# Performance work log

Measured on AMD Instinct MI355X. Metric: run time of the kernel, lower is better.

## Reference

```python
import jax, jax.numpy as jnp
import numpy as np

TOP_K = 2


def setup_inputs() -> dict:
    key = jax.random.key(0)
    k1, k2, k3, k4, k5 = jax.random.split(key, 5)
    B, S, H, F, E = 2, 2048, 1024, 4096, 8
    scale = 0.02
    return {
        "hidden_states": jax.random.normal(k1, (B, S, H), dtype=jnp.float32),
        "w_gate": jax.random.normal(k2, (H, E), dtype=jnp.float32) * scale,
        "w_gate_proj": jax.random.normal(k3, (E, H, F), dtype=jnp.float32) * scale,
        "w_up_proj": jax.random.normal(k4, (E, H, F), dtype=jnp.float32) * scale,
        "w_down_proj": jax.random.normal(k5, (E, F, H), dtype=jnp.float32) * scale,
    }


def reference(hidden_states, w_gate, w_gate_proj, w_up_proj, w_down_proj):
    B, S, H = hidden_states.shape
    E = w_gate_proj.shape[0]
    x = hidden_states.reshape(-1, H)  # [T, H]

    # Router: softmax in float32, then top-k (NOT renormalized, matching source).
    router_logits = x @ w_gate  # [T, E]
    routing_probs = jax.nn.softmax(router_logits.astype(jnp.float32), axis=-1)
    routing_weights, selected_experts = jax.lax.top_k(routing_probs, TOP_K)  # [T, k]
    routing_weights = routing_weights.astype(x.dtype)

    out = jnp.zeros_like(x)
    # Small fixed loop over experts; per-token weight is zero for unrouted
    # tokens, so the masked dense computation is mathematically identical to
    # the gather/index_add dispatch in the source.
    for e in range(E):
        w_e = jnp.sum(routing_weights * (selected_experts == e), axis=-1)  # [T]
        h = jax.nn.silu(x @ w_gate_proj[e]) * (x @ w_up_proj[e])  # [T, F]
        out = out + (h @ w_down_proj[e]) * w_e[:, None]
    return out.reshape(B, S, H)
```

## Files before the change

### kernel.cpp

```cpp
#include <hip/hip_runtime.h>
#include <hip/hip_bf16.h>

#define T_TOK 4096
#define HDIM  1024
#define FDIM  4096
#define NEXP  8
#define CAP   4096
#define NTMAX 64
#define OBR   8192

typedef __attribute__((ext_vector_type(8))) short short8;
typedef __attribute__((ext_vector_type(4))) float floatx4;
typedef __attribute__((ext_vector_type(4))) float float4v;
typedef __attribute__((ext_vector_type(4))) unsigned short ushort4v;

__device__ __forceinline__ unsigned short f2bf(float f) {
    union { float f; unsigned int u; } v; v.f = f;
    unsigned int u = v.u;
    u += 0x7fffu + ((u >> 16) & 1u);
    return (unsigned short)(u >> 16);
}

__device__ __forceinline__ void gl2lds16(const void* g, void* l) {
    __builtin_amdgcn_global_load_lds(
        (const __attribute__((address_space(1))) unsigned int*)g,
        (__attribute__((address_space(3))) unsigned int*)l,
        16, 0, 0);
}

__global__ void k_transpose_cast(const float* __restrict__ src, unsigned short* __restrict__ dst,
                                 int R, int C) {
    __shared__ float tile[64][65];
    size_t base = (size_t)blockIdx.z * (size_t)R * (size_t)C;
    int c0 = blockIdx.x * 64, r0 = blockIdx.y * 64;
    int lx = threadIdx.x & 15, ly = threadIdx.x >> 4;
#pragma unroll
    for (int i = 0; i < 4; ++i) {
        int rr = i * 16 + ly;
        float4v v = *(const float4v*)(src + base + (size_t)(r0 + rr) * C + c0 + lx * 4);
        tile[rr][lx * 4 + 0] = v[0]; tile[rr][lx * 4 + 1] = v[1];
        tile[rr][lx * 4 + 2] = v[2]; tile[rr][lx * 4 + 3] = v[3];
    }
    __syncthreads();
#pragma unroll
    for (int i = 0; i < 4; ++i) {
        int cc = i * 16 + ly;
        ushort4v o = { f2bf(tile[lx * 4 + 0][cc]), f2bf(tile[lx * 4 + 1][cc]),
                       f2bf(tile[lx * 4 + 2][cc]), f2bf(tile[lx * 4 + 3][cc]) };
        *(ushort4v*)(dst + base + (size_t)(c0 + cc) * R + r0 + lx * 4) = o;
    }
}

__global__ void k_transpose_cast2(const float* __restrict__ s0, const float* __restrict__ s1,
                                  unsigned short* __restrict__ d0, unsigned short* __restrict__ d1) {
    const int R = HDIM, C = FDIM;
    __shared__ float tile[64][65];
    int m = blockIdx.z >> 3, zz = blockIdx.z & 7;
    const float* src = (m ? s1 : s0);
    unsigned short* dst = (m ? d1 : d0);
    size_t base = (size_t)zz * (size_t)R * (size_t)C;
    int c0 = blockIdx.x * 64, r0 = blockIdx.y * 64;
    int lx = threadIdx.x & 15, ly = threadIdx.x >> 4;
#pragma unroll
    for (int i = 0; i < 4; ++i) {
        int rr = i * 16 + ly;
        float4v v = *(const float4v*)(src + base + (size_t)(r0 + rr) * C + c0 + lx * 4);
        tile[rr][lx * 4 + 0] = v[0]; tile[rr][lx * 4 + 1] = v[1];
        tile[rr][lx * 4 + 2] = v[2]; tile[rr][lx * 4 + 3] = v[3];
    }
    __syncthreads();
#pragma unroll
    for (int i = 0; i < 4; ++i) {
        int cc = i * 16 + ly;
        ushort4v o = { f2bf(tile[lx * 4 + 0][cc]), f2bf(tile[lx * 4 + 1][cc]),
                       f2bf(tile[lx * 4 + 2][cc]), f2bf(tile[lx * 4 + 3][cc]) };
        *(ushort4v*)(dst + base + (size_t)(c0 + cc) * R + r0 + lx * 4) = o;
    }
}

__global__ void k_router(const float* __restrict__ x, const float* __restrict__ wgate,
                         unsigned short* __restrict__ xb,
                         int* __restrict__ counts, int* __restrict__ ltok,
                         float* __restrict__ lwt, int* __restrict__ tslot) {
    int lane = threadIdx.x & 63;
    int tok = blockIdx.x * 4 + (threadIdx.x >> 6);
    const float* xr = x + (size_t)tok * HDIM;
    unsigned short* xbr = xb + (size_t)tok * HDIM;
    float acc[NEXP];
#pragma unroll
    for (int e = 0; e < NEXP; ++e) acc[e] = 0.f;
    for (int it = 0; it < HDIM / 256; ++it) {
        int h0 = it * 256 + lane * 4;
        float4v xv = *(const float4v*)(xr + h0);
        ushort4v xo = { f2bf(xv[0]), f2bf(xv[1]), f2bf(xv[2]), f2bf(xv[3]) };
        *(ushort4v*)(xbr + h0) = xo;
#pragma unroll
        for (int j = 0; j < 4; ++j) {
            float4v w0 = *(const float4v*)(wgate + (size_t)(h0 + j) * NEXP);
            float4v w1 = *(const float4v*)(wgate + (size_t)(h0 + j) * NEXP + 4);
            float xs = xv[j];
            acc[0] += xs * w0[0]; acc[1] += xs * w0[1];
            acc[2] += xs * w0[2]; acc[3] += xs * w0[3];
            acc[4] += xs * w1[0]; acc[5] += xs * w1[1];
            acc[6] += xs * w1[2]; acc[7] += xs * w1[3];
        }
    }
#pragma unroll
    for (int off = 32; off >= 1; off >>= 1)
#pragma unroll
        for (int e = 0; e < NEXP; ++e)
            acc[e] += __shfl_xor(acc[e], off, 64);
    if (lane == 0) {
        float m = acc[0];
#pragma unroll
        for (int e = 1; e < NEXP; ++e) m = fmaxf(m, acc[e]);
        float p[NEXP], s = 0.f;
#pragma unroll
        for (int e = 0; e < NEXP; ++e) { p[e] = __expf(acc[e] - m); s += p[e]; }
        float inv = 1.f / s;
#pragma unroll
        for (int e = 0; e < NEXP; ++e) p[e] *= inv;
        int e0 = 0; float b0 = p[0];
#pragma unroll
        for (int e = 1; e < NEXP; ++e) if (p[e] > b0) { b0 = p[e]; e0 = e; }
        int e1 = -1; float b1 = -1.f;
#pragma unroll
        for (int e = 0; e < NEXP; ++e) if (e != e0 && p[e] > b1) { b1 = p[e]; e1 = e; }
        int p0 = atomicAdd(&counts[e0], 1);
        ltok[e0 * CAP + p0] = tok; lwt[e0 * CAP + p0] = b0;
        int p1 = atomicAdd(&counts[e1], 1);
        ltok[e1 * CAP + p1] = tok; lwt[e1 * CAP + p1] = b1;
        tslot[tok * 2]     = (e0 << 16) | p0;
        tslot[tok * 2 + 1] = (e1 << 16) | p1;
    }
}

__global__ void k_prefix(const int* __restrict__ counts, int* __restrict__ offs,
                         int* __restrict__ wl, int* __restrict__ nwl) {
    if (threadIdx.x == 0) {
        int s = 0;
#pragma unroll
        for (int e = 0; e < NEXP; ++e) { offs[e] = s; s += counts[e]; }
        int n = 0;
        for (int e = 0; e < NEXP; ++e)
            for (int r = 0; r * 256 < counts[e] && n < NTMAX; ++r)
                wl[n++] = (e << 8) | r;
        nwl[0] = n;
    }
}

__global__ __launch_bounds__(512, 4)
void k_gemm1(const unsigned short* __restrict__ xb,
             const unsigned short* __restrict__ wgt,
             const unsigned short* __restrict__ wut,
             const int* __restrict__ counts, const int* __restrict__ offs,
             const int* __restrict__ ltok,
             const int* __restrict__ wl, const int* __restrict__ nwl,
             unsigned short* __restrict__ hbuf)
{
    const int bid = blockIdx.x;
    const int ftile = bid & 63;
    const int by = bid >> 6;
    if (by >= nwl[0]) return;
    const int w = wl[by];
    const int e = w >> 8, rowtile = w & 255;
    const int M = counts[e];

    __shared__ __align__(16) unsigned short lA[2][256 * 32];
    __shared__ __align__(16) unsigned short lBg[2][64 * 32];
    __shared__ __align__(16) unsigned short lBu[2][64 * 32];
    __shared__ int stok[256];

    const int t = threadIdx.x;
    const int wv = t >> 6, lane = t & 63;

    if (t < 256) {
        int i = rowtile * 256 + t;
        stok[t] = (i < M) ? ltok[e * CAP + i] : ltok[e * CAP];
    }
    __syncthreads();

    const int srow = wv * 16 + (lane >> 2);
    const int k4 = lane & 3;
    const int swA = (k4 ^ ((srow >> 1) & 3)) * 8;
    const unsigned short* pA0 = xb + (size_t)stok[srow] * HDIM + swA;
    const unsigned short* pA1 = xb + (size_t)stok[128 + srow] * HDIM + swA;
    const int brow = (wv & 3) * 16 + (lane >> 2);
    const int swB = (k4 ^ ((brow >> 1) & 3)) * 8;
    const unsigned short* wsrc = (wv < 4) ? wgt : wut;
    const unsigned short* pB = wsrc + ((size_t)e * FDIM + ftile * 64 + brow) * HDIM + swB;

    const int wm = wv >> 1, wn = wv & 1;
    const int fr = lane & 15, kg = lane >> 4;
    const int cswz = (kg ^ ((fr >> 1) & 3)) * 8;

    floatx4 accg[4][2], accu[4][2];
#pragma unroll
    for (int mi = 0; mi < 4; ++mi)
#pragma unroll
        for (int ni = 0; ni < 2; ++ni) {
            floatx4 z = {0.f, 0.f, 0.f, 0.f};
            accg[mi][ni] = z; accu[mi][ni] = z;
        }

    auto stage = [&](int b) {
        gl2lds16(pA0, &lA[b][wv * 512]);        pA0 += 32;
        gl2lds16(pA1, &lA[b][4096 + wv * 512]); pA1 += 32;
        gl2lds16(pB, (wv < 4) ? &lBg[b][(wv & 3) * 512]
                              : &lBu[b][(wv & 3) * 512]);
        pB += 32;
    };
    auto compute = [&](int b) {
        short8 a[4], g[2], u[2];
#pragma unroll
        for (int mi = 0; mi < 4; ++mi)
            a[mi] = *(const short8*)&lA[b][(wm * 64 + mi * 16 + fr) * 32 + cswz];
#pragma unroll
        for (int ni = 0; ni < 2; ++ni) {
            g[ni] = *(const short8*)&lBg[b][(wn * 32 + ni * 16 + fr) * 32 + cswz];
            u[ni] = *(const short8*)&lBu[b][(wn * 32 + ni * 16 + fr) * 32 + cswz];
        }
#pragma unroll
        for (int mi = 0; mi < 4; ++mi)
#pragma unroll
            for (int ni = 0; ni < 2; ++ni) {
                accg[mi][ni] = __builtin_amdgcn_mfma_f32_16x16x32_bf16(a[mi], g[ni], accg[mi][ni], 0, 0, 0);
                accu[mi][ni] = __builtin_amdgcn_mfma_f32_16x16x32_bf16(a[mi], u[ni], accu[mi][ni], 0, 0, 0);
            }
    };

    stage(0);
    __syncthreads();
#pragma unroll 1
    for (int it = 0; it < 16; ++it) {
        stage(1);
        compute(0);
        __syncthreads();
        if (it < 15) stage(0);
        compute(1);
        __syncthreads();
    }

    const int hrow0 = offs[e] + rowtile * 256;
#pragma unroll
    for (int mi = 0; mi < 4; ++mi)
#pragma unroll
        for (int ni = 0; ni < 2; ++ni) {
            int c = ftile * 64 + wn * 32 + ni * 16 + fr;
#pragma unroll
            for (int r = 0; r < 4; ++r) {
                int rr = wm * 64 + mi * 16 + kg * 4 + r;
                if (rowtile * 256 + rr < M) {
                    float g = accg[mi][ni][r];
                    float val = (g / (1.f + __expf(-g))) * accu[mi][ni][r];
                    hbuf[(size_t)(hrow0 + rr) * FDIM + c] = f2bf(val);
                }
            }
        }
}

__global__ __launch_bounds__(512, 4)
void k_gemm2(const unsigned short* __restrict__ hbuf,
             const unsigned short* __restrict__ wdt,
             const int* __restrict__ counts, const int* __restrict__ offs,
             const float* __restrict__ lwt,
             const int* __restrict__ wl, const int* __restrict__ nwl,
             float* __restrict__ obuf)
{
    const int bid = blockIdx.x;
    const int htile = bid & 7;
    const int kq = (bid >> 3) & 3;
    const int by = bid >> 5;
    if (by >= nwl[0]) return;
    const int w = wl[by];
    const int e = w >> 8, rowtile = w & 255;
    const int M = counts[e];

    __shared__ __align__(16) unsigned short lA[2][256 * 32];
    __shared__ __align__(16) unsigned short lB[2][128 * 32];
    __shared__ float swt[256];

    const int t = threadIdx.x;
    const int wv = t >> 6, lane = t & 63;

    if (t < 256) {
        int i = rowtile * 256 + t;
        swt[t] = (i < M) ? lwt[e * CAP + i] : 0.f;
    }

    const int row0 = offs[e] + rowtile * 256;
    const int srow = wv * 16 + (lane >> 2);
    const int k4 = lane & 3;
    const int sw = (k4 ^ ((srow >> 1) & 3)) * 8;
    const int kofs = kq * (FDIM / 4);
    const int ra0 = min(row0 + srow, OBR - 1);
    const int ra1 = min(row0 + 128 + srow, OBR - 1);
    const unsigned short* pA0 = hbuf + (size_t)ra0 * FDIM + kofs + sw;
    const unsigned short* pA1 = hbuf + (size_t)ra1 * FDIM + kofs + sw;
    const unsigned short* pB = wdt + ((size_t)e * HDIM + htile * 128 + srow) * FDIM + kofs + sw;

    const int wm = wv >> 1, wn = wv & 1;
    const int fr = lane & 15, kg = lane >> 4;
    const int cswz = (kg ^ ((fr >> 1) & 3)) * 8;

    floatx4 acc[4][4];
#pragma unroll
    for (int mi = 0; mi < 4; ++mi)
#pragma unroll
        for (int ni = 0; ni < 4; ++ni) {
            floatx4 z = {0.f, 0.f, 0.f, 0.f};
            acc[mi][ni] = z;
        }

    auto stage = [&](int b) {
        gl2lds16(pA0, &lA[b][wv * 512]);        pA0 += 32;
        gl2lds16(pA1, &lA[b][4096 + wv * 512]); pA1 += 32;
        gl2lds16(pB,  &lB[b][wv * 512]);        pB += 32;
    };
    auto compute = [&](int b) {
        short8 a[4], bb[4];
#pragma unroll
        for (int mi = 0; mi < 4; ++mi)
            a[mi] = *(const short8*)&lA[b][(wm * 64 + mi * 16 + fr) * 32 + cswz];
#pragma unroll
        for (int ni = 0; ni < 4; ++ni)
            bb[ni] = *(const short8*)&lB[b][(wn * 64 + ni * 16 + fr) * 32 + cswz];
#pragma unroll
        for (int mi = 0; mi < 4; ++mi)
#pragma unroll
            for (int ni = 0; ni < 4; ++ni)
                acc[mi][ni] = __builtin_amdgcn_mfma_f32_16x16x32_bf16(a[mi], bb[ni], acc[mi][ni], 0, 0, 0);
    };

    stage(0);
    __syncthreads();
#pragma unroll 1
    for (int it = 0; it < 16; ++it) {
        stage(1);
        compute(0);
        __syncthreads();
        if (it < 15) stage(0);
        compute(1);
        __syncthreads();
    }

    float* ob = obuf + (size_t)kq * OBR * HDIM;
#pragma unroll
    for (int mi = 0; mi < 4; ++mi)
#pragma unroll
        for (int ni = 0; ni < 4; ++ni) {
            int c = htile * 128 + wn * 64 + ni * 16 + fr;
#pragma unroll
            for (int r = 0; r < 4; ++r) {
                int rr = wm * 64 + mi * 16 + kg * 4 + r;
                if (rowtile * 256 + rr < M)
                    ob[(size_t)(row0 + rr) * HDIM + c] = acc[mi][ni][r] * swt[rr];
            }
        }
}

__global__ void k_combine(const float* __restrict__ obuf, const int* __restrict__ tslot,
                          const int* __restrict__ offs, float* __restrict__ out) {
    int gid = blockIdx.x * 256 + threadIdx.x;
    int tok = gid >> 8;
    int c = (gid & 255) * 4;
    int s0 = tslot[tok * 2], s1 = tslot[tok * 2 + 1];
    size_t r0 = (size_t)(offs[s0 >> 16] + (s0 & 0xFFFF));
    size_t r1 = (size_t)(offs[s1 >> 16] + (s1 & 0xFFFF));
    float4v s = {0.f, 0.f, 0.f, 0.f};
#pragma unroll
    for (int q = 0; q < 4; ++q) {
        s += *(const float4v*)(obuf + ((size_t)q * OBR + r0) * HDIM + c);
        s += *(const float4v*)(obuf + ((size_t)q * OBR + r1) * HDIM + c);
    }
    *(float4v*)(out + (size_t)tok * HDIM + c) = s;
}

extern "C" void kernel_launch(void* const* d_in, const int* in_sizes, int n_in,
                              void* d_out, int out_size, void* d_ws, size_t ws_size,
                              hipStream_t stream) {
    const float* x     = (const float*)d_in[0];
    const float* wgate = (const float*)d_in[1];
    const float* wg    = (const float*)d_in[2];
    const float* wu    = (const float*)d_in[3];
    const float* wd    = (const float*)d_in[4];
    float* out = (float*)d_out;

    char* ws = (char*)d_ws;
    size_t off = 0;
    unsigned short* xb  = (unsigned short*)(ws + off); off += (size_t)T_TOK * HDIM * 2;
    unsigned short* wgt = (unsigned short*)(ws + off); off += (size_t)NEXP * FDIM * HDIM * 2;
    unsigned short* wut = (unsigned short*)(ws + off); off += (size_t)NEXP * FDIM * HDIM * 2;
    unsigned short* wdt = (unsigned short*)(ws + off); off += (size_t)NEXP * HDIM * FDIM * 2;
    unsigned short* hbuf= (unsigned short*)(ws + off); off += (size_t)OBR * FDIM * 2;
    int*   ltok   = (int*)(ws + off);   off += (size_t)NEXP * CAP * 4;
    float* lwt    = (float*)(ws + off); off += (size_t)NEXP * CAP * 4;
    int*   tslot  = (int*)(ws + off);   off += (size_t)T_TOK * 2 * 4;
    int*   counts = (int*)(ws + off);   off += 256;
    int*   offs   = (int*)(ws + off);   off += 256;
    int*   wl     = (int*)(ws + off);   off += NTMAX * 4;
    int*   nwl    = (int*)(ws + off);   off += 256;
    float* obuf = (float*)wgt;

    hipMemsetAsync(counts, 0, 32, stream);

    k_router<<<T_TOK / 4, 256, 0, stream>>>(x, wgate, xb, counts, ltok, lwt, tslot);
    k_transpose_cast2<<<dim3(FDIM / 64, HDIM / 64, 16), 256, 0, stream>>>(wg, wu, wgt, wut);
    k_transpose_cast<<<dim3(HDIM / 64, FDIM / 64, NEXP), 256, 0, stream>>>(wd, wdt, FDIM, HDIM);
    k_prefix<<<1, 64, 0, stream>>>(counts, offs, wl, nwl);
    k_gemm1<<<64 * 40, 512, 0, stream>>>(xb, wgt, wut, counts, offs, ltok, wl, nwl, hbuf);
    k_gemm2<<<32 * 40, 512, 0, stream>>>(hbuf, wdt, counts, offs, lwt, wl, nwl, obuf);
    k_combine<<<T_TOK * HDIM / 1024, 256, 0, stream>>>(obuf, tslot, offs, out);
}
```

Baseline: 827.6 us.

## Fuse fp32 weight cast and transpose into GEMM B-tile staging

```diff
diff --git a/kernel.cpp b/kernel.cpp
--- a/kernel.cpp
+++ b/kernel.cpp
@@ -12,6 +12,7 @@
 typedef __attribute__((ext_vector_type(8))) short short8;
 typedef __attribute__((ext_vector_type(4))) float floatx4;
 typedef __attribute__((ext_vector_type(4))) float float4v;
+typedef __attribute__((ext_vector_type(2))) float float2v;
 typedef __attribute__((ext_vector_type(4))) unsigned short ushort4v;
 
 __device__ __forceinline__ unsigned short f2bf(float f) {
@@ -26,56 +27,6 @@
         (const __attribute__((address_space(1))) unsigned int*)g,
         (__attribute__((address_space(3))) unsigned int*)l,
         16, 0, 0);
-}
-
-__global__ void k_transpose_cast(const float* __restrict__ src, unsigned short* __restrict__ dst,
-                                 int R, int C) {
-    __shared__ float tile[64][65];
-    size_t base = (size_t)blockIdx.z * (size_t)R * (size_t)C;
-    int c0 = blockIdx.x * 64, r0 = blockIdx.y * 64;
-    int lx = threadIdx.x & 15, ly = threadIdx.x >> 4;
-#pragma unroll
-    for (int i = 0; i < 4; ++i) {
-        int rr = i * 16 + ly;
-        float4v v = *(const float4v*)(src + base + (size_t)(r0 + rr) * C + c0 + lx * 4);
-        tile[rr][lx * 4 + 0] = v[0]; tile[rr][lx * 4 + 1] = v[1];
-        tile[rr][lx * 4 + 2] = v[2]; tile[rr][lx * 4 + 3] = v[3];
-    }
-    __syncthreads();
-#pragma unroll
-    for (int i = 0; i < 4; ++i) {
-        int cc = i * 16 + ly;
-        ushort4v o = { f2bf(tile[lx * 4 + 0][cc]), f2bf(tile[lx * 4 + 1][cc]),
-                       f2bf(tile[lx * 4 + 2][cc]), f2bf(tile[lx * 4 + 3][cc]) };
-        *(ushort4v*)(dst + base + (size_t)(c0 + cc) * R + r0 + lx * 4) = o;
-    }
-}
-
-__global__ void k_transpose_cast2(const float* __restrict__ s0, const float* __restrict__ s1,
-                                  unsigned short* __restrict__ d0, unsigned short* __restrict__ d1) {
-    const int R = HDIM, C = FDIM;
-    __shared__ float tile[64][65];
-    int m = blockIdx.z >> 3, zz = blockIdx.z & 7;
-    const float* src = (m ? s1 : s0);
-    unsigned short* dst = (m ? d1 : d0);
-    size_t base = (size_t)zz * (size_t)R * (size_t)C;
-    int c0 = blockIdx.x * 64, r0 = blockIdx.y * 64;
-    int lx = threadIdx.x & 15, ly = threadIdx.x >> 4;
-#pragma unroll
-    for (int i = 0; i < 4; ++i) {
-        int rr = i * 16 + ly;
-        float4v v = *(const float4v*)(src + base + (size_t)(r0 + rr) * C + c0 + lx * 4);
-        tile[rr][lx * 4 + 0] = v[0]; tile[rr][lx * 4 + 1] = v[1];
-        tile[rr][lx * 4 + 2] = v[2]; tile[rr][lx * 4 + 3] = v[3];
-    }
-    __syncthreads();
-#pragma unroll
-    for (int i = 0; i < 4; ++i) {
-        int cc = i * 16 + ly;
-        ushort4v o = { f2bf(tile[lx * 4 + 0][cc]), f2bf(tile[lx * 4 + 1][cc]),
-                       f2bf(tile[lx * 4 + 2][cc]), f2bf(tile[lx * 4 + 3][cc]) };
-        *(ushort4v*)(dst + base + (size_t)(c0 + cc) * R + r0 + lx * 4) = o;
-    }
 }
 
 __global__ void k_router(const float* __restrict__ x, const float* __restrict__ wgate,
@@ -151,8 +102,8 @@
 
 __global__ __launch_bounds__(512, 4)
 void k_gemm1(const unsigned short* __restrict__ xb,
-             const unsigned short* __restrict__ wgt,
-             const unsigned short* __restrict__ wut,
+             const float* __restrict__ wg,
+             const float* __restrict__ wu,
              const int* __restrict__ counts, const int* __restrict__ offs,
              const int* __restrict__ ltok,
              const int* __restrict__ wl, const int* __restrict__ nwl,
@@ -185,10 +136,13 @@
     const int swA = (k4 ^ ((srow >> 1) & 3)) * 8;
     const unsigned short* pA0 = xb + (size_t)stok[srow] * HDIM + swA;
     const unsigned short* pA1 = xb + (size_t)stok[128 + srow] * HDIM + swA;
-    const int brow = (wv & 3) * 16 + (lane >> 2);
-    const int swB = (k4 ^ ((brow >> 1) & 3)) * 8;
-    const unsigned short* wsrc = (wv < 4) ? wgt : wut;
-    const unsigned short* pB = wsrc + ((size_t)e * FDIM + ftile * 64 + brow) * HDIM + swB;
+
+    const int tt = t & 255;
+    const int bn0 = 2 * (tt & 31);
+    const int bk0 = 4 * (tt >> 5);
+    const float* wsrc = (wv < 4) ? wg : wu;
+    const float* pB = wsrc + (size_t)e * HDIM * FDIM + (size_t)bk0 * FDIM + ftile * 64 + bn0;
+    const int wo0 = bn0 * 32 + (((bk0 >> 3) ^ ((bn0 >> 1) & 3)) << 3) + (bk0 & 7);
 
     const int wm = wv >> 1, wn = wv & 1;
     const int fr = lane & 15, kg = lane >> 4;
@@ -203,12 +157,24 @@
             accg[mi][ni] = z; accu[mi][ni] = z;
         }
 
-    auto stage = [&](int b) {
+    float2v q0, q1, q2, q3;
+    auto ldB = [&]() {
+        q0 = *(const float2v*)(pB);
+        q1 = *(const float2v*)(pB + FDIM);
+        q2 = *(const float2v*)(pB + 2 * FDIM);
+        q3 = *(const float2v*)(pB + 3 * FDIM);
+        pB += 32 * FDIM;
+    };
+    auto writeB = [&](int b) {
+        unsigned short* base = ((wv < 4) ? &lBg[b][0] : &lBu[b][0]) + wo0;
+        ushort4v lo = { f2bf(q0[0]), f2bf(q1[0]), f2bf(q2[0]), f2bf(q3[0]) };
+        ushort4v hi = { f2bf(q0[1]), f2bf(q1[1]), f2bf(q2[1]), f2bf(q3[1]) };
+        *(ushort4v*)(base) = lo;
+        *(ushort4v*)(base + 32) = hi;
+    };
+    auto stageA = [&](int b) {
         gl2lds16(pA0, &lA[b][wv * 512]);        pA0 += 32;
         gl2lds16(pA1, &lA[b][4096 + wv * 512]); pA1 += 32;
-        gl2lds16(pB, (wv < 4) ? &lBg[b][(wv & 3) * 512]
-                              : &lBu[b][(wv & 3) * 512]);
-        pB += 32;
     };
     auto compute = [&](int b) {
         short8 a[4], g[2], u[2];
@@ -229,15 +195,17 @@
             }
     };
 
-    stage(0);
+    ldB();
+    stageA(0);
+    writeB(0);
     __syncthreads();
+
 #pragma unroll 1
-    for (int it = 0; it < 16; ++it) {
-        stage(1);
-        compute(0);
-        __syncthreads();
-        if (it < 15) stage(0);
-        compute(1);
+    for (int it = 0; it < 32; ++it) {
+        const int b = it & 1;
+        if (it < 31) { ldB(); stageA(b ^ 1); }
+        compute(b);
+        if (it < 31) writeB(b ^ 1);
         __syncthreads();
     }
 
@@ -261,7 +229,7 @@
 
 __global__ __launch_bounds__(512, 4)
 void k_gemm2(const unsigned short* __restrict__ hbuf,
-             const unsigned short* __restrict__ wdt,
+             const float* __restrict__ wd,
              const int* __restrict__ counts, const int* __restrict__ offs,
              const float* __restrict__ lwt,
              const int* __restrict__ wl, const int* __restrict__ nwl,
@@ -289,15 +257,20 @@
     }
 
     const int row0 = offs[e] + rowtile * 256;
+
     const int srow = wv * 16 + (lane >> 2);
     const int k4 = lane & 3;
-    const int sw = (k4 ^ ((srow >> 1) & 3)) * 8;
+    const int swA = (k4 ^ ((srow >> 1) & 3)) * 8;
     const int kofs = kq * (FDIM / 4);
     const int ra0 = min(row0 + srow, OBR - 1);
     const int ra1 = min(row0 + 128 + srow, OBR - 1);
-    const unsigned short* pA0 = hbuf + (size_t)ra0 * FDIM + kofs + sw;
-    const unsigned short* pA1 = hbuf + (size_t)ra1 * FDIM + kofs + sw;
-    const unsigned short* pB = wdt + ((size_t)e * HDIM + htile * 128 + srow) * FDIM + kofs + sw;
+    const unsigned short* pA0 = hbuf + (size_t)ra0 * FDIM + kofs + swA;
+    const unsigned short* pA1 = hbuf + (size_t)ra1 * FDIM + kofs + swA;
+
+    const int bn0 = 2 * (t & 63);
+    const int bk0 = 4 * wv;
+    const float* pB = wd + (size_t)e * FDIM * HDIM + (size_t)(kofs + bk0) * HDIM + htile * 128 + bn0;
+    const int wo0 = bn0 * 32 + (((bk0 >> 3) ^ ((bn0 >> 1) & 3)) << 3) + (bk0 & 7);
 
     const int wm = wv >> 1, wn = wv & 1;
     const int fr = lane & 15, kg = lane >> 4;
@@ -312,10 +285,24 @@
             acc[mi][ni] = z;
         }
 
-    auto stage = [&](int b) {
+    float2v q0, q1, q2, q3;
+    auto ldB = [&]() {
+        q0 = *(const float2v*)(pB);
+        q1 = *(const float2v*)(pB + HDIM);
+        q2 = *(const float2v*)(pB + 2 * HDIM);
+        q3 = *(const float2v*)(pB + 3 * HDIM);
+        pB += 32 * HDIM;
+    };
+    auto writeB = [&](int b) {
+        unsigned short* base = &lB[b][0] + wo0;
+        ushort4v lo = { f2bf(q0[0]), f2bf(q1[0]), f2bf(q2[0]), f2bf(q3[0]) };
+        ushort4v hi = { f2bf(q0[1]), f2bf(q1[1]), f2bf(q2[1]), f2bf(q3[1]) };
+        *(ushort4v*)(base) = lo;
+        *(ushort4v*)(base + 32) = hi;
+    };
+    auto stageA = [&](int b) {
         gl2lds16(pA0, &lA[b][wv * 512]);        pA0 += 32;
         gl2lds16(pA1, &lA[b][4096 + wv * 512]); pA1 += 32;
-        gl2lds16(pB,  &lB[b][wv * 512]);        pB += 32;
     };
     auto compute = [&](int b) {
         short8 a[4], bb[4];
@@ -332,15 +319,17 @@
                 acc[mi][ni] = __builtin_amdgcn_mfma_f32_16x16x32_bf16(a[mi], bb[ni], acc[mi][ni], 0, 0, 0);
     };
 
-    stage(0);
+    ldB();
+    stageA(0);
+    writeB(0);
     __syncthreads();
+
 #pragma unroll 1
-    for (int it = 0; it < 16; ++it) {
-        stage(1);
-        compute(0);
-        __syncthreads();
-        if (it < 15) stage(0);
-        compute(1);
+    for (int it = 0; it < 32; ++it) {
+        const int b = it & 1;
+        if (it < 31) { ldB(); stageA(b ^ 1); }
+        compute(b);
+        if (it < 31) writeB(b ^ 1);
         __syncthreads();
     }
 
@@ -389,10 +378,8 @@
     char* ws = (char*)d_ws;
     size_t off = 0;
     unsigned short* xb  = (unsigned short*)(ws + off); off += (size_t)T_TOK * HDIM * 2;
-    unsigned short* wgt = (unsigned short*)(ws + off); off += (size_t)NEXP * FDIM * HDIM * 2;
-    unsigned short* wut = (unsigned short*)(ws + off); off += (size_t)NEXP * FDIM * HDIM * 2;
-    unsigned short* wdt = (unsigned short*)(ws + off); off += (size_t)NEXP * HDIM * FDIM * 2;
     unsigned short* hbuf= (unsigned short*)(ws + off); off += (size_t)OBR * FDIM * 2;
+    float* obuf = (float*)(ws + off);   off += (size_t)4 * OBR * HDIM * 4;
     int*   ltok   = (int*)(ws + off);   off += (size_t)NEXP * CAP * 4;
     float* lwt    = (float*)(ws + off); off += (size_t)NEXP * CAP * 4;
     int*   tslot  = (int*)(ws + off);   off += (size_t)T_TOK * 2 * 4;
@@ -400,15 +387,12 @@
     int*   offs   = (int*)(ws + off);   off += 256;
     int*   wl     = (int*)(ws + off);   off += NTMAX * 4;
     int*   nwl    = (int*)(ws + off);   off += 256;
-    float* obuf = (float*)wgt;
 
     hipMemsetAsync(counts, 0, 32, stream);
 
     k_router<<<T_TOK / 4, 256, 0, stream>>>(x, wgate, xb, counts, ltok, lwt, tslot);
-    k_transpose_cast2<<<dim3(FDIM / 64, HDIM / 64, 16), 256, 0, stream>>>(wg, wu, wgt, wut);
-    k_transpose_cast<<<dim3(HDIM / 64, FDIM / 64, NEXP), 256, 0, stream>>>(wd, wdt, FDIM, HDIM);
     k_prefix<<<1, 64, 0, stream>>>(counts, offs, wl, nwl);
-    k_gemm1<<<64 * 40, 512, 0, stream>>>(xb, wgt, wut, counts, offs, ltok, wl, nwl, hbuf);
-    k_gemm2<<<32 * 40, 512, 0, stream>>>(hbuf, wdt, counts, offs, lwt, wl, nwl, obuf);
+    k_gemm1<<<64 * 40, 512, 0, stream>>>(xb, wg, wu, counts, offs, ltok, wl, nwl, hbuf);
+    k_gemm2<<<32 * 40, 512, 0, stream>>>(hbuf, wd, counts, offs, lwt, wl, nwl, obuf);
     k_combine<<<T_TOK * HDIM / 1024, 256, 0, stream>>>(obuf, tslot, offs, out);
 }
```

Result: no change. 832.8 us (+0.6%).
